# Kernel optimization log

Hardware: AMD Instinct MI355X
Metric: run time of the kernel (lower is better)

## Reference

```python
import jax, jax.numpy as jnp
import numpy as np

N_LEVELS = 16
F = 2                      # n_features_per_level
LOG2_HASHMAP = 19
TABLE_SIZE = 1 << LOG2_HASHMAP
BASE_RES = 16.0
FINEST_RES = 512.0
BOX_MIN, BOX_MAX = -1.0, 1.0
PRIMES = jnp.array([1, 2654435761, 805459861], dtype=jnp.uint32)
# corner offsets, i outer / k inner, matching BOX_OFFSETS_3D ordering
OFFSETS = jnp.array([[i, j, k] for i in (0, 1) for j in (0, 1) for k in (0, 1)], dtype=jnp.int32)  # [8,3]


def _hash(coords):
    # coords: int32 [N,8,3]; torch int32 mul wraps mod 2^32 -> emulate with uint32
    c = coords.astype(jnp.uint32)
    h = (c[..., 0] * PRIMES[0]) ^ (c[..., 1] * PRIMES[1]) ^ (c[..., 2] * PRIMES[2])
    return (h & jnp.uint32(TABLE_SIZE - 1)).astype(jnp.int32)


def setup_inputs() -> dict:
    key = jax.random.key(0)
    k1, k2 = jax.random.split(key)
    x = jax.random.uniform(k1, (1_000_000, 3), dtype=jnp.float32) * 2.0 - 1.0  # inside [-1,1]^3
    # nn.init.uniform_(w, -1e-4, 1e-4)
    tables = (jax.random.uniform(k2, (N_LEVELS, TABLE_SIZE, F), dtype=jnp.float32) * 2.0 - 1.0) * 1e-4
    return {"x": x, "tables": tables}


def reference(x, tables):
    n = x.shape[0]
    b = jnp.exp((jnp.log(FINEST_RES) - jnp.log(BASE_RES)) / (N_LEVELS - 1))
    resolutions = jnp.floor(BASE_RES * b ** jnp.arange(N_LEVELS, dtype=jnp.float32))  # [L]
    xc = jnp.clip(x, BOX_MIN, BOX_MAX)

    def level(res, table):
        grid = (BOX_MAX - BOX_MIN) / res                      # scalar
        bl = jnp.floor((xc - BOX_MIN) / grid).astype(jnp.int32)  # [N,3] bottom-left voxel idx
        vmin = bl.astype(jnp.float32) * grid + BOX_MIN        # [N,3]
        idx = bl[:, None, :] + OFFSETS                        # [N,8,3]
        emb = table[_hash(idx)]                               # [N,8,F] irregular gather
        # weights use original (unclamped) x, as in the torch forward
        w = (x - vmin) / grid                                 # [N,3]
        e = emb.reshape(n, 2, 2, 2, F)
        e = e[:, 0] * (1 - w[:, 0, None, None, None]) + e[:, 1] * w[:, 0, None, None, None]  # [N,2,2,F]
        e = e[:, 0] * (1 - w[:, 1, None, None]) + e[:, 1] * w[:, 1, None, None]              # [N,2,F]
        e = e[:, 0] * (1 - w[:, 2, None]) + e[:, 1] * w[:, 2, None]                          # [N,F]
        return e

    out = jax.vmap(level)(resolutions, tables)  # [L,N,F]
    # torch.cat(x_embedded_all, dim=-1): level-major feature layout
    return jnp.transpose(out, (1, 0, 2)).reshape(n, N_LEVELS * F)
```

## Files before the change

kernel.cpp:

```cpp
#include <hip/hip_runtime.h>
#include <cmath>

#define NL 16
#define NPAIR 7
#define TABLE_SIZE (1u << 19)
#define TABLE_MASK (TABLE_SIZE - 1u)
#define P1 2654435761u
#define P2 805459861u

typedef float f2v __attribute__((ext_vector_type(2)));
typedef float f4v __attribute__((ext_vector_type(4)));
typedef unsigned long long u64;

struct Params {
  float g[NL];
  int R[NPAIR];
  unsigned off[NPAIR];
  unsigned nE[NPAIR];
  unsigned totE;
};

__device__ __forceinline__ f2v ld_agent(const f2v* p) {
  u64 raw = __hip_atomic_load((const u64*)p, __ATOMIC_RELAXED, __HIP_MEMORY_SCOPE_AGENT);
  union { u64 u; f2v f; } c; c.u = raw; return c.f;
}

struct Corners { unsigned idx[8]; float wx, wy, wz; };

__device__ __forceinline__ Corners make_corners(
    float g, float px, float py, float pz, float qx, float qy, float qz)
{
  Corners c;
  const float fx = floorf((qx + 1.f) / g);
  const float fy = floorf((qy + 1.f) / g);
  const float fz = floorf((qz + 1.f) / g);
  c.wx = (px - (fx * g - 1.f)) / g;
  c.wy = (py - (fy * g - 1.f)) / g;
  c.wz = (pz - (fz * g - 1.f)) / g;
  const unsigned hx0 = (unsigned)(int)fx;
  const unsigned hy0 = (unsigned)(int)fy * P1;
  const unsigned hz0 = (unsigned)(int)fz * P2;
  const unsigned hx1 = hx0 + 1u;
  const unsigned hy1 = hy0 + P1;
  const unsigned hz1 = hz0 + P2;
  c.idx[0] = (hx0 ^ hy0 ^ hz0) & TABLE_MASK;
  c.idx[1] = (hx0 ^ hy0 ^ hz1) & TABLE_MASK;
  c.idx[2] = (hx0 ^ hy1 ^ hz0) & TABLE_MASK;
  c.idx[3] = (hx0 ^ hy1 ^ hz1) & TABLE_MASK;
  c.idx[4] = (hx1 ^ hy0 ^ hz0) & TABLE_MASK;
  c.idx[5] = (hx1 ^ hy0 ^ hz1) & TABLE_MASK;
  c.idx[6] = (hx1 ^ hy1 ^ hz0) & TABLE_MASK;
  c.idx[7] = (hx1 ^ hy1 ^ hz1) & TABLE_MASK;
  return c;
}

__device__ __forceinline__ f2v trilerp(const f2v e[8], float wx, float wy, float wz) {
  const float ux = 1.f - wx;
  const f2v a00 = e[0] * ux + e[4] * wx;
  const f2v a01 = e[1] * ux + e[5] * wx;
  const f2v a10 = e[2] * ux + e[6] * wx;
  const f2v a11 = e[3] * ux + e[7] * wx;
  const float uy = 1.f - wy;
  const f2v b0 = a00 * uy + a10 * wy;
  const f2v b1 = a01 * uy + a11 * wy;
  const float uz = 1.f - wz;
  return b0 * uz + b1 * wz;
}

__device__ __forceinline__ f2v pair_eval(
    const f4v* __restrict__ pt, int R, float g,
    float px, float py, float pz, float qx, float qy, float qz)
{
  const float fx = floorf((qx + 1.f) / g);
  const float fy = floorf((qy + 1.f) / g);
  const float fz = floorf((qz + 1.f) / g);
  const float wx = (px - (fx * g - 1.f)) / g;
  const float wy = (py - (fy * g - 1.f)) / g;
  const float wz = (pz - (fz * g - 1.f)) / g;
  const int bx = (int)fx, by = (int)fy, bz = (int)fz;
  const int s = R + 1;
  const int base = (bx * (R + 2) + by) * s + bz;
  const f4v p00 = pt[base];
  const f4v p01 = pt[base + s];
  const f4v p10 = pt[base + (R + 2) * s];
  const f4v p11 = pt[base + (R + 3) * s];
  const float uz = 1.f - wz;
  const f2v a00 = { p00[0] * uz + p00[2] * wz, p00[1] * uz + p00[3] * wz };
  const f2v a01 = { p01[0] * uz + p01[2] * wz, p01[1] * uz + p01[3] * wz };
  const f2v a10 = { p10[0] * uz + p10[2] * wz, p10[1] * uz + p10[3] * wz };
  const f2v a11 = { p11[0] * uz + p11[2] * wz, p11[1] * uz + p11[3] * wz };
  const float uy = 1.f - wy;
  const f2v b0 = a00 * uy + a01 * wy;
  const f2v b1 = a10 * uy + a11 * wy;
  const float ux = 1.f - wx;
  return b0 * ux + b1 * wx;
}

__global__ __launch_bounds__(256) void rehash_kernel(
    const float* __restrict__ tables, f4v* __restrict__ pt, Params P)
{
  unsigned tid = blockIdx.x * 256 + threadIdx.x;
  if (tid >= P.totE) return;
  int l = 0; unsigned e = tid;
  while (e >= P.nE[l]) { e -= P.nE[l]; ++l; }
  const unsigned R = (unsigned)P.R[l];
  const unsigned vz = e % (R + 1u);
  const unsigned t2 = e / (R + 1u);
  const unsigned vy = t2 % (R + 2u);
  const unsigned vx = t2 / (R + 2u);
  const f2v* tab = (const f2v*)tables + (size_t)l * TABLE_SIZE;
  const unsigned h0 = (vx ^ (vy * P1) ^ (vz * P2)) & TABLE_MASK;
  const unsigned h1 = (vx ^ (vy * P1) ^ ((vz + 1u) * P2)) & TABLE_MASK;
  const f2v a = tab[h0], b = tab[h1];
  const f4v o = { a[0], a[1], b[0], b[1] };
  pt[P.off[l] + e] = o;
}

__global__ __launch_bounds__(256) void coarse_pass_kernel(
    const float* __restrict__ xin, const f4v* __restrict__ pt,
    f2v* __restrict__ ws, int npts, Params P)
{
  const int n = blockIdx.x * 256 + threadIdx.x;
  if (n >= npts) return;
  const float px = __builtin_nontemporal_load(&xin[3 * n + 0]);
  const float py = __builtin_nontemporal_load(&xin[3 * n + 1]);
  const float pz = __builtin_nontemporal_load(&xin[3 * n + 2]);
  const float qx = fminf(fmaxf(px, -1.f), 1.f);
  const float qy = fminf(fmaxf(py, -1.f), 1.f);
  const float qz = fminf(fmaxf(pz, -1.f), 1.f);
#pragma unroll
  for (int l = 0; l < 5; ++l) {
    const f2v r = pair_eval(pt + P.off[l], P.R[l], P.g[l], px, py, pz, qx, qy, qz);
    __builtin_nontemporal_store(r, ws + (size_t)l * npts + n);
  }
}

__global__ __launch_bounds__(256) void pair_pass_kernel(
    const float* __restrict__ xin, const f4v* __restrict__ pt,
    f2v* __restrict__ wsl, int npts, int strideT, int R, float g)
{
  const int n0 = blockIdx.x * 256 + threadIdx.x;
  const int n1 = n0 + strideT;
  const int c0 = n0 < npts ? n0 : npts - 1;
  const int c1 = n1 < npts ? n1 : npts - 1;
  const float px0 = xin[3 * c0 + 0], py0 = xin[3 * c0 + 1], pz0 = xin[3 * c0 + 2];
  const float px1 = xin[3 * c1 + 0], py1 = xin[3 * c1 + 1], pz1 = xin[3 * c1 + 2];
  const float qx0 = fminf(fmaxf(px0, -1.f), 1.f), qy0 = fminf(fmaxf(py0, -1.f), 1.f), qz0 = fminf(fmaxf(pz0, -1.f), 1.f);
  const float qx1 = fminf(fmaxf(px1, -1.f), 1.f), qy1 = fminf(fmaxf(py1, -1.f), 1.f), qz1 = fminf(fmaxf(pz1, -1.f), 1.f);
  const f2v r0 = pair_eval(pt, R, g, px0, py0, pz0, qx0, qy0, qz0);
  const f2v r1 = pair_eval(pt, R, g, px1, py1, pz1, qx1, qy1, qz1);
  if (n0 < npts) __builtin_nontemporal_store(r0, wsl + n0);
  if (n1 < npts) __builtin_nontemporal_store(r1, wsl + n1);
}

__global__ __launch_bounds__(256) void fine_pass_kernel(
    const float* __restrict__ xin, const f2v* __restrict__ tab,
    f2v* __restrict__ wsl, int npts, int strideT, float g)
{
  const int nb = blockIdx.x * 256 + threadIdx.x;
  int n[4], c[4];
#pragma unroll
  for (int i = 0; i < 4; ++i) {
    n[i] = nb + i * strideT;
    c[i] = n[i] < npts ? n[i] : npts - 1;
  }
  Corners cr[4];
#pragma unroll
  for (int i = 0; i < 4; ++i) {
    const float px = xin[3 * c[i] + 0], py = xin[3 * c[i] + 1], pz = xin[3 * c[i] + 2];
    const float qx = fminf(fmaxf(px, -1.f), 1.f);
    const float qy = fminf(fmaxf(py, -1.f), 1.f);
    const float qz = fminf(fmaxf(pz, -1.f), 1.f);
    cr[i] = make_corners(g, px, py, pz, qx, qy, qz);
  }
  f2v e[4][8];
#pragma unroll
  for (int i = 0; i < 4; ++i)
#pragma unroll
    for (int j = 0; j < 8; ++j) e[i][j] = ld_agent(tab + cr[i].idx[j]);
#pragma unroll
  for (int i = 0; i < 4; ++i) {
    const f2v r = trilerp(e[i], cr[i].wx, cr[i].wy, cr[i].wz);
    if (n[i] < npts) __builtin_nontemporal_store(r, wsl + n[i]);
  }
}

__global__ __launch_bounds__(256) void transpose_kernel(
    const f2v* __restrict__ ws, float* __restrict__ out, int npts)
{
  __shared__ f2v lds[NL][257];
  const int t = threadIdx.x;
  const int base = blockIdx.x * 256;
  const int n = base + t;
  if (n < npts) {
#pragma unroll
    for (int l = 0; l < NL; ++l)
      lds[l][t] = __builtin_nontemporal_load(ws + (size_t)l * npts + n);
  }
  __syncthreads();
#pragma unroll
  for (int k = 0; k < 8; ++k) {
    const int j4 = t + 256 * k;
    const int p = j4 >> 3;
    const int lp = j4 & 7;
    if (base + p < npts) {
      const f2v a = lds[2 * lp + 0][p];
      const f2v b = lds[2 * lp + 1][p];
      const f4v v = { a[0], a[1], b[0], b[1] };
      __builtin_nontemporal_store(v, (f4v*)(out + (size_t)base * 32) + j4);
    }
  }
}

__global__ __launch_bounds__(256) void hash_embed_fused_kernel(
    const float* __restrict__ xin, const float* __restrict__ tables,
    float* __restrict__ out, int npts, Params P)
{
  int n = blockIdx.x * blockDim.x + threadIdx.x;
  if (n >= npts) return;
  const float px = xin[3 * n + 0], py = xin[3 * n + 1], pz = xin[3 * n + 2];
  const float qx = fminf(fmaxf(px, -1.f), 1.f);
  const float qy = fminf(fmaxf(py, -1.f), 1.f);
  const float qz = fminf(fmaxf(pz, -1.f), 1.f);
  f2v acc[NL];
#pragma unroll
  for (int l = 0; l < NL; ++l) {
    const Corners c = make_corners(P.g[l], px, py, pz, qx, qy, qz);
    const f2v* tab = (const f2v*)tables + (size_t)l * TABLE_SIZE;
    f2v e[8];
#pragma unroll
    for (int j = 0; j < 8; ++j) e[j] = tab[c.idx[j]];
    acc[l] = trilerp(e, c.wx, c.wy, c.wz);
  }
  f4v* o = (f4v*)(out + (size_t)n * 32);
#pragma unroll
  for (int i = 0; i < 8; ++i) {
    const f4v v = { acc[2 * i][0], acc[2 * i][1], acc[2 * i + 1][0], acc[2 * i + 1][1] };
    o[i] = v;
  }
}

extern "C" void kernel_launch(void* const* d_in, const int* in_sizes, int n_in,
                              void* d_out, int out_size, void* d_ws, size_t ws_size,
                              hipStream_t stream) {
  const float* x = (const float*)d_in[0];
  const float* tables = (const float*)d_in[1];
  float* out = (float*)d_out;
  const int npts = in_sizes[0] / 3;

  Params P;
  {
    const float b = expf((logf(512.0f) - logf(16.0f)) / 15.0f);
    unsigned off = 0;
    for (int l = 0; l < NL; ++l) {
      const float r = floorf(16.0f * powf(b, (float)l));
      P.g[l] = 2.0f / r;
      if (l < NPAIR) {
        const int R = (int)r;
        P.R[l] = R;
        P.nE[l] = (unsigned)((R + 2) * (R + 2) * (R + 1));
        P.off[l] = off;
        off += P.nE[l];
      }
    }
    P.totE = off;
  }

  const size_t ws_needed = (size_t)NL * npts * sizeof(f2v);
  const size_t pair_bytes = (size_t)P.totE * sizeof(f4v);
  const size_t out_bytes = (size_t)out_size * sizeof(float);

  if (ws_size >= ws_needed && out_bytes >= pair_bytes) {
    f2v* ws = (f2v*)d_ws;
    f4v* pt = (f4v*)d_out;

    hipLaunchKernelGGL(rehash_kernel, dim3((P.totE + 255) / 256), dim3(256), 0, stream,
                       tables, pt, P);

    hipLaunchKernelGGL(coarse_pass_kernel, dim3((npts + 255) / 256), dim3(256), 0, stream,
                       x, pt, ws, npts, P);

    const int grid2 = (npts + 511) / 512;
    const int stride2 = grid2 * 256;
    for (int l = 5; l < NPAIR; ++l)
      hipLaunchKernelGGL(pair_pass_kernel, dim3(grid2), dim3(256), 0, stream,
                         x, pt + P.off[l], ws + (size_t)l * npts, npts, stride2,
                         P.R[l], P.g[l]);

    const int grid4 = (npts + 1023) / 1024;
    const int stride4 = grid4 * 256;
    for (int l = NPAIR; l < NL; ++l)
      hipLaunchKernelGGL(fine_pass_kernel, dim3(grid4), dim3(256), 0, stream,
                         x, (const f2v*)tables + (size_t)l * TABLE_SIZE,
                         ws + (size_t)l * npts, npts, stride4, P.g[l]);

    hipLaunchKernelGGL(transpose_kernel, dim3((npts + 255) / 256), dim3(256), 0, stream,
                       ws, out, npts);
  } else {
    hipLaunchKernelGGL(hash_embed_fused_kernel, dim3((npts + 255) / 256), dim3(256), 0, stream,
                       x, tables, out, npts, P);
  }
}
```

Before: 520.4 us.

## Fuse finest level into final transpose and extend pair tables to more levels

The finest level's hash lookup and trilinear interpolation now run inside the final transpose kernel. Its result goes straight to shared memory, which removes one workspace write and read pass and one kernel launch. NPAIR rises from 7 to 9, so levels 7 and 8 also use the z-pair-packed tables and need 4 loads of 16 bytes instead of 8 random loads. In exchange, the pre-built pair tables grow larger and add rehash work and cache footprint. Some type aliases and a helper were renamed.

```diff
diff --git a/kernel.cpp b/kernel.cpp
--- a/kernel.cpp
+++ b/kernel.cpp
@@ -2,7 +2,7 @@
 #include <cmath>
 
 #define NL 16
-#define NPAIR 7
+#define NPAIR 9
 #define TABLE_SIZE (1u << 19)
 #define TABLE_MASK (TABLE_SIZE - 1u)
 #define P1 2654435761u
@@ -10,14 +10,15 @@
 
 typedef float f2v __attribute__((ext_vector_type(2)));
 typedef float f4v __attribute__((ext_vector_type(4)));
+typedef unsigned int u32;
 typedef unsigned long long u64;
 
 struct Params {
   float g[NL];
   int R[NPAIR];
-  unsigned off[NPAIR];
-  unsigned nE[NPAIR];
-  unsigned totE;
+  u32 off[NPAIR];
+  u32 nE[NPAIR];
+  u32 totE;
 };
 
 __device__ __forceinline__ f2v ld_agent(const f2v* p) {
@@ -25,7 +26,7 @@
   union { u64 u; f2v f; } c; c.u = raw; return c.f;
 }
 
-struct Corners { unsigned idx[8]; float wx, wy, wz; };
+struct Corners { u32 idx[8]; float wx, wy, wz; };
 
 __device__ __forceinline__ Corners make_corners(
     float g, float px, float py, float pz, float qx, float qy, float qz)
@@ -37,12 +38,12 @@
   c.wx = (px - (fx * g - 1.f)) / g;
   c.wy = (py - (fy * g - 1.f)) / g;
   c.wz = (pz - (fz * g - 1.f)) / g;
-  const unsigned hx0 = (unsigned)(int)fx;
-  const unsigned hy0 = (unsigned)(int)fy * P1;
-  const unsigned hz0 = (unsigned)(int)fz * P2;
-  const unsigned hx1 = hx0 + 1u;
-  const unsigned hy1 = hy0 + P1;
-  const unsigned hz1 = hz0 + P2;
+  const u32 hx0 = (u32)(int)fx;
+  const u32 hy0 = (u32)(int)fy * P1;
+  const u32 hz0 = (u32)(int)fz * P2;
+  const u32 hx1 = hx0 + 1u;
+  const u32 hy1 = hy0 + P1;
+  const u32 hz1 = hz0 + P2;
   c.idx[0] = (hx0 ^ hy0 ^ hz0) & TABLE_MASK;
   c.idx[1] = (hx0 ^ hy0 ^ hz1) & TABLE_MASK;
   c.idx[2] = (hx0 ^ hy1 ^ hz0) & TABLE_MASK;
@@ -54,7 +55,7 @@
   return c;
 }
 
-__device__ __forceinline__ f2v trilerp(const f2v e[8], float wx, float wy, float wz) {
+__device__ __forceinline__ f2v trilerp8(const f2v e[8], float wx, float wy, float wz) {
   const float ux = 1.f - wx;
   const f2v a00 = e[0] * ux + e[4] * wx;
   const f2v a01 = e[1] * ux + e[5] * wx;
@@ -99,18 +100,18 @@
 __global__ __launch_bounds__(256) void rehash_kernel(
     const float* __restrict__ tables, f4v* __restrict__ pt, Params P)
 {
-  unsigned tid = blockIdx.x * 256 + threadIdx.x;
+  u32 tid = blockIdx.x * 256 + threadIdx.x;
   if (tid >= P.totE) return;
-  int l = 0; unsigned e = tid;
+  int l = 0; u32 e = tid;
   while (e >= P.nE[l]) { e -= P.nE[l]; ++l; }
-  const unsigned R = (unsigned)P.R[l];
-  const unsigned vz = e % (R + 1u);
-  const unsigned t2 = e / (R + 1u);
-  const unsigned vy = t2 % (R + 2u);
-  const unsigned vx = t2 / (R + 2u);
+  const u32 R = (u32)P.R[l];
+  const u32 vz = e % (R + 1u);
+  const u32 t2 = e / (R + 1u);
+  const u32 vy = t2 % (R + 2u);
+  const u32 vx = t2 / (R + 2u);
   const f2v* tab = (const f2v*)tables + (size_t)l * TABLE_SIZE;
-  const unsigned h0 = (vx ^ (vy * P1) ^ (vz * P2)) & TABLE_MASK;
-  const unsigned h1 = (vx ^ (vy * P1) ^ ((vz + 1u) * P2)) & TABLE_MASK;
+  const u32 h0 = (vx ^ (vy * P1) ^ (vz * P2)) & TABLE_MASK;
+  const u32 h1 = (vx ^ (vy * P1) ^ ((vz + 1u) * P2)) & TABLE_MASK;
   const f2v a = tab[h0], b = tab[h1];
   const f4v o = { a[0], a[1], b[0], b[1] };
   pt[P.off[l] + e] = o;
@@ -180,22 +181,32 @@
     for (int j = 0; j < 8; ++j) e[i][j] = ld_agent(tab + cr[i].idx[j]);
 #pragma unroll
   for (int i = 0; i < 4; ++i) {
-    const f2v r = trilerp(e[i], cr[i].wx, cr[i].wy, cr[i].wz);
+    const f2v r = trilerp8(e[i], cr[i].wx, cr[i].wy, cr[i].wz);
     if (n[i] < npts) __builtin_nontemporal_store(r, wsl + n[i]);
   }
 }
 
-__global__ __launch_bounds__(256) void transpose_kernel(
-    const f2v* __restrict__ ws, float* __restrict__ out, int npts)
+__global__ __launch_bounds__(256) void final_kernel(
+    const float* __restrict__ xin, const f2v* __restrict__ tab15,
+    const f2v* __restrict__ ws, float* __restrict__ out, int npts, float g15)
 {
   __shared__ f2v lds[NL][257];
   const int t = threadIdx.x;
   const int base = blockIdx.x * 256;
   const int n = base + t;
   if (n < npts) {
-#pragma unroll
-    for (int l = 0; l < NL; ++l)
+    const float px = xin[3 * n + 0], py = xin[3 * n + 1], pz = xin[3 * n + 2];
+    const float qx = fminf(fmaxf(px, -1.f), 1.f);
+    const float qy = fminf(fmaxf(py, -1.f), 1.f);
+    const float qz = fminf(fmaxf(pz, -1.f), 1.f);
+    const Corners c = make_corners(g15, px, py, pz, qx, qy, qz);
+    f2v e[8];
+#pragma unroll
+    for (int j = 0; j < 8; ++j) e[j] = ld_agent(tab15 + c.idx[j]);
+#pragma unroll
+    for (int l = 0; l < NL - 1; ++l)
       lds[l][t] = __builtin_nontemporal_load(ws + (size_t)l * npts + n);
+    lds[NL - 1][t] = trilerp8(e, c.wx, c.wy, c.wz);
   }
   __syncthreads();
 #pragma unroll
@@ -230,7 +241,7 @@
     f2v e[8];
 #pragma unroll
     for (int j = 0; j < 8; ++j) e[j] = tab[c.idx[j]];
-    acc[l] = trilerp(e, c.wx, c.wy, c.wz);
+    acc[l] = trilerp8(e, c.wx, c.wy, c.wz);
   }
   f4v* o = (f4v*)(out + (size_t)n * 32);
 #pragma unroll
@@ -251,14 +262,14 @@
   Params P;
   {
     const float b = expf((logf(512.0f) - logf(16.0f)) / 15.0f);
-    unsigned off = 0;
+    u32 off = 0;
     for (int l = 0; l < NL; ++l) {
       const float r = floorf(16.0f * powf(b, (float)l));
       P.g[l] = 2.0f / r;
       if (l < NPAIR) {
         const int R = (int)r;
         P.R[l] = R;
-        P.nE[l] = (unsigned)((R + 2) * (R + 2) * (R + 1));
+        P.nE[l] = (u32)((R + 2) * (R + 2) * (R + 1));
         P.off[l] = off;
         off += P.nE[l];
       }
@@ -266,7 +277,7 @@
     P.totE = off;
   }
 
-  const size_t ws_needed = (size_t)NL * npts * sizeof(f2v);
+  const size_t ws_needed = (size_t)(NL - 1) * npts * sizeof(f2v);
   const size_t pair_bytes = (size_t)P.totE * sizeof(f4v);
   const size_t out_bytes = (size_t)out_size * sizeof(float);
 
@@ -277,7 +288,8 @@
     hipLaunchKernelGGL(rehash_kernel, dim3((P.totE + 255) / 256), dim3(256), 0, stream,
                        tables, pt, P);
 
-    hipLaunchKernelGGL(coarse_pass_kernel, dim3((npts + 255) / 256), dim3(256), 0, stream,
+    const int grid = (npts + 255) / 256;
+    hipLaunchKernelGGL(coarse_pass_kernel, dim3(grid), dim3(256), 0, stream,
                        x, pt, ws, npts, P);
 
     const int grid2 = (npts + 511) / 512;
@@ -289,13 +301,14 @@
 
     const int grid4 = (npts + 1023) / 1024;
     const int stride4 = grid4 * 256;
-    for (int l = NPAIR; l < NL; ++l)
+    for (int l = NPAIR; l < NL - 1; ++l)
       hipLaunchKernelGGL(fine_pass_kernel, dim3(grid4), dim3(256), 0, stream,
                          x, (const f2v*)tables + (size_t)l * TABLE_SIZE,
                          ws + (size_t)l * npts, npts, stride4, P.g[l]);
 
-    hipLaunchKernelGGL(transpose_kernel, dim3((npts + 255) / 256), dim3(256), 0, stream,
-                       ws, out, npts);
+    hipLaunchKernelGGL(final_kernel, dim3(grid), dim3(256), 0, stream,
+                       x, (const f2v*)tables + (size_t)15 * TABLE_SIZE,
+                       ws, out, npts, P.g[15]);
   } else {
     hipLaunchKernelGGL(hash_embed_fused_kernel, dim3((npts + 255) / 256), dim3(256), 0, stream,
                        x, tables, out, npts, P);
```

New measurement: 565.0 us. 1.09x slower.
